# Kernel optimization log

Hardware: AMD Instinct MI355X
Metric: run time of the kernel (lower is better)

Reference implementation:

```python
import jax, jax.numpy as jnp
import numpy as np

NUM_EXPERTS_PER_TOK = 2

def setup_inputs() -> dict:
    key = jax.random.key(0)
    k1, k2, k3, k4 = jax.random.split(key, 4)
    B, S, D, O, E = 2, 4096, 2048, 2048, 8
    x = jax.random.normal(k1, (B, S, D), dtype=jnp.float32)
    gate_w = jax.random.normal(k2, (E, D), dtype=jnp.float32) * 0.02
    expert_w = jax.random.normal(k3, (E, O, D), dtype=jnp.float32) * 0.02
    expert_b = jax.random.normal(k4, (E, O), dtype=jnp.float32) * 0.02
    return {"x": x, "gate_w": gate_w, "expert_w": expert_w, "expert_b": expert_b}

def reference(x, gate_w, expert_w, expert_b):
    E = gate_w.shape[0]
    O = expert_w.shape[1]
    # Router: gate logits [B,S,E], top-k selection, softmax over the k logits (fp32 then cast)
    gate_logits = jnp.einsum('bsd,ed->bse', x, gate_w)
    topk_vals, topk_idx = jax.lax.top_k(gate_logits, NUM_EXPERTS_PER_TOK)
    weights = jax.nn.softmax(topk_vals.astype(jnp.float32), axis=-1).astype(x.dtype)
    # Dense combine weights [B,S,E]: weight of expert e for each token (0 if not selected)
    dense_w = jnp.sum(jax.nn.one_hot(topk_idx, E, dtype=x.dtype) * weights[..., None], axis=2)
    # Per-expert linear + weighted combine (loop over small fixed E)
    out = jnp.zeros(x.shape[:2] + (O,), dtype=x.dtype)
    for e in range(E):
        y_e = jnp.einsum('bsd,od->bso', x, expert_w[e]) + expert_b[e]
        out = out + dense_w[..., e:e + 1] * y_e
    return out
```

## Files before the change

### kernel.cpp

```cpp
#include <hip/hip_runtime.h>
#include <stdint.h>
#include <math.h>

#define T_TOK 8192
#define DIM   2048
#define OUTD  2048
#define NEXP  8
#define NKT   (DIM / 32)

typedef __bf16 bf16x8 __attribute__((ext_vector_type(8)));
typedef float  f32x4  __attribute__((ext_vector_type(4)));

__device__ __forceinline__ unsigned short f2bf(float f) {
  union { float f; uint32_t u; } c = {f};
  uint32_t r = (c.u + 0x7FFFu + ((c.u >> 16) & 1u)) >> 16;
  return (unsigned short)r;
}
__device__ __forceinline__ float bf2f(unsigned short h) {
  union { uint32_t u; float f; } c = {((uint32_t)h) << 16};
  return c.f;
}

__device__ __forceinline__ void gld_lds16(const void* g, void* l) {
  auto gp = reinterpret_cast<const __attribute__((address_space(1))) char*>(
      reinterpret_cast<uintptr_t>(g));
  auto lp = reinterpret_cast<__attribute__((address_space(3))) char*>(
      reinterpret_cast<uintptr_t>(l));
  __builtin_amdgcn_global_load_lds(gp, lp, 16, 0, 0);
}

__global__ __launch_bounds__(256) void split_hi_lo(const float* __restrict__ src,
                                                   unsigned short* __restrict__ hi,
                                                   unsigned short* __restrict__ lo,
                                                   int n4) {
  int stride = gridDim.x * blockDim.x;
  for (int i = blockIdx.x * blockDim.x + threadIdx.x; i < n4; i += stride) {
    float4 v = reinterpret_cast<const float4*>(src)[i];
    ushort4 h, l;
    h.x = f2bf(v.x); l.x = f2bf(v.x - bf2f(h.x));
    h.y = f2bf(v.y); l.y = f2bf(v.y - bf2f(h.y));
    h.z = f2bf(v.z); l.z = f2bf(v.z - bf2f(h.z));
    h.w = f2bf(v.w); l.w = f2bf(v.w - bf2f(h.w));
    reinterpret_cast<ushort4*>(hi)[i] = h;
    reinterpret_cast<ushort4*>(lo)[i] = l;
  }
}

__global__ __launch_bounds__(256) void router_split(const float* __restrict__ x,
                                                    const float* __restrict__ gw,
                                                    unsigned short* __restrict__ xh,
                                                    unsigned short* __restrict__ xl,
                                                    int* __restrict__ cnt,
                                                    int* __restrict__ tok_list,
                                                    float* __restrict__ tok_w) {
  const int t    = blockIdx.x * 4 + (threadIdx.x >> 6);
  const int lane = threadIdx.x & 63;
  const float4* xr = reinterpret_cast<const float4*>(x + (size_t)t * DIM);
  ushort4* xhr = reinterpret_cast<ushort4*>(xh + (size_t)t * DIM);
  ushort4* xlr = reinterpret_cast<ushort4*>(xl + (size_t)t * DIM);
  double acc[NEXP];
#pragma unroll
  for (int e = 0; e < NEXP; ++e) acc[e] = 0.0;
#pragma unroll
  for (int i = 0; i < DIM / (4 * 64); ++i) {
    float4 xv = xr[i * 64 + lane];
    ushort4 h, l;
    h.x = f2bf(xv.x); l.x = f2bf(xv.x - bf2f(h.x));
    h.y = f2bf(xv.y); l.y = f2bf(xv.y - bf2f(h.y));
    h.z = f2bf(xv.z); l.z = f2bf(xv.z - bf2f(h.z));
    h.w = f2bf(xv.w); l.w = f2bf(xv.w - bf2f(h.w));
    xhr[i * 64 + lane] = h;
    xlr[i * 64 + lane] = l;
#pragma unroll
    for (int e = 0; e < NEXP; ++e) {
      float4 gv = reinterpret_cast<const float4*>(gw + e * DIM)[i * 64 + lane];
      acc[e] += (double)xv.x * gv.x + (double)xv.y * gv.y +
                (double)xv.z * gv.z + (double)xv.w * gv.w;
    }
  }
#pragma unroll
  for (int off = 32; off >= 1; off >>= 1)
#pragma unroll
    for (int e = 0; e < NEXP; ++e) acc[e] += __shfl_down(acc[e], off, 64);
  if (lane == 0) {
    float lg[NEXP];
#pragma unroll
    for (int e = 0; e < NEXP; ++e) lg[e] = (float)acc[e];
    int i0 = 0; float v0 = lg[0];
    int i1 = -1; float v1 = -3.4e38f;
#pragma unroll
    for (int e = 1; e < NEXP; ++e) {
      if (lg[e] > v0)      { i1 = i0; v1 = v0; i0 = e; v0 = lg[e]; }
      else if (lg[e] > v1) { i1 = e;  v1 = lg[e]; }
    }
    float p  = expf(v1 - v0);
    float w0 = 1.0f / (1.0f + p);
    float w1 = p * w0;
    int s0 = atomicAdd(&cnt[i0], 1);
    tok_list[i0 * T_TOK + s0] = t; tok_w[i0 * T_TOK + s0] = w0;
    int s1 = atomicAdd(&cnt[i1], 1);
    tok_list[i1 * T_TOK + s1] = t; tok_w[i1 * T_TOK + s1] = w1;
  }
}

__global__ __launch_bounds__(512, 2) void moe_gemm(
    const unsigned short* __restrict__ xh, const unsigned short* __restrict__ xl,
    const unsigned short* __restrict__ wh, const unsigned short* __restrict__ wl,
    const float* __restrict__ eb,
    const int* __restrict__ cnt,
    const int* __restrict__ tok_list, const float* __restrict__ tok_w,
    float* __restrict__ out) {
  const int gid = blockIdx.x;
  const int by  = gid & 7;
  const int rb  = gid >> 3;
  int e = 0, off = 0, ce = 0;
#pragma unroll
  for (int ee = 0; ee < NEXP; ++ee) {
    int c  = cnt[ee];
    int nb = (c + 255) >> 8;
    if (rb >= off && rb < off + nb && ce == 0) { e = ee; ce = c; }
    off += (rb >= off + nb && ce == 0) ? nb : 0;
  }
  if (ce == 0) return;
  const int bx = rb - off;

  const int tid = threadIdx.x;
  const int l   = tid & 63;
  const int w   = tid >> 6;
  const int wr  = w >> 2, wc = w & 3;

  extern __shared__ char smem[];
  int*   stok = reinterpret_cast<int*>(smem + 131072);
  float* sw   = reinterpret_cast<float*>(smem + 132096);

  if (tid < 256) {
    int rg = bx * 256 + tid;
    bool v = rg < ce;
    stok[tid] = v ? tok_list[e * T_TOK + rg] : 0;
    sw[tid]   = v ? tok_w[e * T_TOK + rg]   : 0.0f;
  }
  __syncthreads();

  const unsigned short* asrc[4];
  const unsigned short* bsrc[4];
#pragma unroll
  for (int i = 0; i < 4; ++i) {
    int g = i * 512 + tid;
    int r = g >> 3, p = g & 7, s = p ^ (r & 7);
    asrc[i] = (s < 4 ? xh : xl) + (size_t)stok[r] * DIM + (s & 3) * 8;
    bsrc[i] = (s < 4 ? wh : wl) + ((size_t)e * OUTD + by * 256 + r) * DIM + (s & 3) * 8;
  }

  const int ph = (l >> 4) ^ (l & 7);
  const int pl = ((l >> 4) + 4) ^ (l & 7);
  const int aOh = (wr * 128 + (l & 15)) * 128 + ph * 16;
  const int aOl = (wr * 128 + (l & 15)) * 128 + pl * 16;
  const int bOh = 32768 + (wc * 64 + (l & 15)) * 128 + ph * 16;
  const int bOl = 32768 + (wc * 64 + (l & 15)) * 128 + pl * 16;

  f32x4 acc[8][4] = {};

  auto STAGE = [&](int buf, int kk) {
    char* base = smem + buf * 65536;
#pragma unroll
    for (int i = 0; i < 4; ++i) {
      gld_lds16(asrc[i] + kk, base + tid * 16 + i * 8192);
      gld_lds16(bsrc[i] + kk, base + 32768 + tid * 16 + i * 8192);
    }
  };

  STAGE(0, 0);

  for (int kt = 0; kt < NKT; ++kt) {
    const int cur = kt & 1;
    if (kt + 1 < NKT) {
      STAGE(cur ^ 1, (kt + 1) * 32);
      asm volatile("s_waitcnt vmcnt(8)" ::: "memory");
    } else {
      asm volatile("s_waitcnt vmcnt(0)" ::: "memory");
    }
    __builtin_amdgcn_s_barrier();
    __builtin_amdgcn_sched_barrier(0);

    char* b = smem + cur * 65536;
    bf16x8 bh[4], bl[4];
#pragma unroll
    for (int n = 0; n < 4; ++n) {
      bh[n] = *reinterpret_cast<const bf16x8*>(b + bOh + n * 2048);
      bl[n] = *reinterpret_cast<const bf16x8*>(b + bOl + n * 2048);
    }
#pragma unroll
    for (int m = 0; m < 8; ++m) {
      bf16x8 ah = *reinterpret_cast<const bf16x8*>(b + aOh + m * 2048);
      bf16x8 al = *reinterpret_cast<const bf16x8*>(b + aOl + m * 2048);
#pragma unroll
      for (int n = 0; n < 4; ++n) {
        acc[m][n] = __builtin_amdgcn_mfma_f32_16x16x32_bf16(ah, bh[n], acc[m][n], 0, 0, 0);
        acc[m][n] = __builtin_amdgcn_mfma_f32_16x16x32_bf16(ah, bl[n], acc[m][n], 0, 0, 0);
        acc[m][n] = __builtin_amdgcn_mfma_f32_16x16x32_bf16(al, bh[n], acc[m][n], 0, 0, 0);
      }
    }
    __builtin_amdgcn_sched_barrier(0);
    __builtin_amdgcn_s_barrier();
  }

#pragma unroll
  for (int n = 0; n < 4; ++n) {
    const int gc = by * 256 + wc * 64 + n * 16 + (l & 15);
    const float bias = eb[e * OUTD + gc];
#pragma unroll
    for (int m = 0; m < 8; ++m) {
      const int r = wr * 128 + m * 16 + (l >> 4) * 4;
#pragma unroll
      for (int q = 0; q < 4; ++q) {
        int   tk = stok[r + q];
        float wt = sw[r + q];
        float val = wt * (acc[m][n][q] + bias);
        atomicAdd(out + (size_t)tk * OUTD + gc, val);
      }
    }
  }
}

__attribute__((constructor)) static void set_lds_attr() {
  hipFuncSetAttribute((const void*)moe_gemm,
                      hipFuncAttributeMaxDynamicSharedMemorySize, 133120);
}

extern "C" void kernel_launch(void* const* d_in, const int* in_sizes, int n_in,
                              void* d_out, int out_size, void* d_ws, size_t ws_size,
                              hipStream_t stream) {
  const float* x  = (const float*)d_in[0];
  const float* gw = (const float*)d_in[1];
  const float* ew = (const float*)d_in[2];
  const float* eb = (const float*)d_in[3];
  float* out = (float*)d_out;

  char* ws = (char*)d_ws;
  int*   cnt      = (int*)(ws);
  int*   tok_list = (int*)(ws + 256);
  float* tok_w    = (float*)(ws + 256 + 262144);
  unsigned short* xh = (unsigned short*)(ws + 524544);
  unsigned short* xl = xh + 16777216;
  unsigned short* wh = xl + 16777216;
  unsigned short* wl = wh + 33554432;

  hipMemsetAsync(cnt, 0, 256, stream);
  hipMemsetAsync(d_out, 0, (size_t)out_size * sizeof(float), stream);

  split_hi_lo<<<4096, 256, 0, stream>>>(ew, wh, wl, 33554432 / 4);
  router_split<<<T_TOK / 4, 256, 0, stream>>>(x, gw, xh, xl, cnt, tok_list, tok_w);

  moe_gemm<<<dim3(576), 512, 133120, stream>>>(xh, xl, wh, wl, eb, cnt,
                                               tok_list, tok_w, out);
}
```

Measured before the change: 1.080 ms.

## Enlarge MoE GEMM row tile to 288 and software-pipeline A-fragment LDS loads

Changes the per-block token tile from 256 to 288 rows (9 m-fragments per wave), shrinking the grid from 576 to 512 blocks so the per-expert work maps more evenly onto the CUs. Global-to-LDS staging now uses 32-bit offsets from one workspace base, and the inner loop prefetches A fragments two steps ahead, with s_setprio raising wave priority around the MFMA bursts. This adds accumulator registers and LDS use (about 141 KB per block), which may reduce occupancy, and the uneven per-wave load count needs different vmcnt waits.

After: 1.014 ms. 6.1% less time.

```diff
diff --git a/kernel.cpp b/kernel.cpp
--- a/kernel.cpp
+++ b/kernel.cpp
@@ -7,6 +7,8 @@
 #define OUTD  2048
 #define NEXP  8
 #define NKT   (DIM / 32)
+#define BM    288
+#define NGRAN (BM * 8 + 2048)
 
 typedef __bf16 bf16x8 __attribute__((ext_vector_type(8)));
 typedef float  f32x4  __attribute__((ext_vector_type(4)));
@@ -117,7 +119,7 @@
 #pragma unroll
   for (int ee = 0; ee < NEXP; ++ee) {
     int c  = cnt[ee];
-    int nb = (c + 255) >> 8;
+    int nb = (c + (BM - 1)) / BM;
     if (rb >= off && rb < off + nb && ce == 0) { e = ee; ce = c; }
     off += (rb >= off + nb && ce == 0) ? nb : 0;
   }
@@ -130,42 +132,52 @@
   const int wr  = w >> 2, wc = w & 3;
 
   extern __shared__ char smem[];
-  int*   stok = reinterpret_cast<int*>(smem + 131072);
-  float* sw   = reinterpret_cast<float*>(smem + 132096);
-
-  if (tid < 256) {
-    int rg = bx * 256 + tid;
+  int*   stok = reinterpret_cast<int*>(smem + 139264);
+  float* sw   = reinterpret_cast<float*>(smem + 140416);
+
+  if (tid < BM) {
+    int rg = bx * BM + tid;
     bool v = rg < ce;
     stok[tid] = v ? tok_list[e * T_TOK + rg] : 0;
     sw[tid]   = v ? tok_w[e * T_TOK + rg]   : 0.0f;
   }
   __syncthreads();
 
-  const unsigned short* asrc[4];
-  const unsigned short* bsrc[4];
-#pragma unroll
-  for (int i = 0; i < 4; ++i) {
+  const char* wsbase = (const char*)xh;
+  uint32_t goff[9];
+#pragma unroll
+  for (int i = 0; i < 9; ++i) {
     int g = i * 512 + tid;
-    int r = g >> 3, p = g & 7, s = p ^ (r & 7);
-    asrc[i] = (s < 4 ? xh : xl) + (size_t)stok[r] * DIM + (s & 3) * 8;
-    bsrc[i] = (s < 4 ? wh : wl) + ((size_t)e * OUTD + by * 256 + r) * DIM + (s & 3) * 8;
-  }
-
-  const int ph = (l >> 4) ^ (l & 7);
-  const int pl = ((l >> 4) + 4) ^ (l & 7);
-  const int aOh = (wr * 128 + (l & 15)) * 128 + ph * 16;
-  const int aOl = (wr * 128 + (l & 15)) * 128 + pl * 16;
-  const int bOh = 32768 + (wc * 64 + (l & 15)) * 128 + ph * 16;
-  const int bOl = 32768 + (wc * 64 + (l & 15)) * 128 + pl * 16;
-
-  f32x4 acc[8][4] = {};
-
-  auto STAGE = [&](int buf, int kk) {
-    char* base = smem + buf * 65536;
-#pragma unroll
-    for (int i = 0; i < 4; ++i) {
-      gld_lds16(asrc[i] + kk, base + tid * 16 + i * 8192);
-      gld_lds16(bsrc[i] + kk, base + 32768 + tid * 16 + i * 8192);
+    if (g < BM * 8) {
+      int r = g >> 3, p = g & 7, s = p ^ (r & 7);
+      goff[i] = (s < 4 ? 0u : 33554432u) +
+                ((uint32_t)stok[r] * DIM + (s & 3) * 8) * 2u;
+    } else if (g < NGRAN) {
+      int gb = g - BM * 8;
+      int r = gb >> 3, p = gb & 7, s = p ^ (r & 7);
+      goff[i] = (s < 4 ? 67108864u : 134217728u) +
+                (((uint32_t)e * OUTD + by * 256 + r) * DIM + (s & 3) * 8) * 2u;
+    } else goff[i] = 0;
+  }
+  __syncthreads();
+
+  const int ph  = (l >> 4) ^ (l & 7);
+  const int pl  = ((l >> 4) + 4) ^ (l & 7);
+  const int aOh = (wr * 144 + (l & 15)) * 128 + ph * 16;
+  const int aOl = (wr * 144 + (l & 15)) * 128 + pl * 16;
+  const int bOh = 36864 + (wc * 64 + (l & 15)) * 128 + ph * 16;
+  const int bOl = 36864 + (wc * 64 + (l & 15)) * 128 + pl * 16;
+
+  f32x4 acc[9][4] = {};
+
+  auto STAGE = [&](int buf, int kt1) {
+    char* base = smem + buf * 69632 + tid * 16;
+    const char* gb = wsbase + kt1 * 64;
+#pragma unroll
+    for (int i = 0; i < 9; ++i) {
+      int g = i * 512 + tid;
+      if (g < NGRAN)
+        gld_lds16(gb + goff[i], base + i * 8192);
     }
   };
 
@@ -174,32 +186,48 @@
   for (int kt = 0; kt < NKT; ++kt) {
     const int cur = kt & 1;
     if (kt + 1 < NKT) {
-      STAGE(cur ^ 1, (kt + 1) * 32);
-      asm volatile("s_waitcnt vmcnt(8)" ::: "memory");
+      STAGE(cur ^ 1, kt + 1);
+      if (w < 4) asm volatile("s_waitcnt vmcnt(9)" ::: "memory");
+      else       asm volatile("s_waitcnt vmcnt(8)" ::: "memory");
     } else {
       asm volatile("s_waitcnt vmcnt(0)" ::: "memory");
     }
     __builtin_amdgcn_s_barrier();
     __builtin_amdgcn_sched_barrier(0);
 
-    char* b = smem + cur * 65536;
-    bf16x8 bh[4], bl[4];
+    const char* b = smem + cur * 69632;
+    auto LD = [&](int o) { return *reinterpret_cast<const bf16x8*>(b + o); };
+
+    bf16x8 bhv[4], blv[4];
 #pragma unroll
     for (int n = 0; n < 4; ++n) {
-      bh[n] = *reinterpret_cast<const bf16x8*>(b + bOh + n * 2048);
-      bl[n] = *reinterpret_cast<const bf16x8*>(b + bOl + n * 2048);
-    }
-#pragma unroll
-    for (int m = 0; m < 8; ++m) {
-      bf16x8 ah = *reinterpret_cast<const bf16x8*>(b + aOh + m * 2048);
-      bf16x8 al = *reinterpret_cast<const bf16x8*>(b + aOl + m * 2048);
+      bhv[n] = LD(bOh + n * 2048);
+      blv[n] = LD(bOl + n * 2048);
+    }
+    auto MM = [&](bf16x8 ah, bf16x8 al, int m) {
 #pragma unroll
       for (int n = 0; n < 4; ++n) {
-        acc[m][n] = __builtin_amdgcn_mfma_f32_16x16x32_bf16(ah, bh[n], acc[m][n], 0, 0, 0);
-        acc[m][n] = __builtin_amdgcn_mfma_f32_16x16x32_bf16(ah, bl[n], acc[m][n], 0, 0, 0);
-        acc[m][n] = __builtin_amdgcn_mfma_f32_16x16x32_bf16(al, bh[n], acc[m][n], 0, 0, 0);
+        acc[m][n] = __builtin_amdgcn_mfma_f32_16x16x32_bf16(ah, bhv[n], acc[m][n], 0, 0, 0);
+        acc[m][n] = __builtin_amdgcn_mfma_f32_16x16x32_bf16(ah, blv[n], acc[m][n], 0, 0, 0);
+        acc[m][n] = __builtin_amdgcn_mfma_f32_16x16x32_bf16(al, bhv[n], acc[m][n], 0, 0, 0);
       }
-    }
+    };
+
+    bf16x8 c0h = LD(aOh),            c0l = LD(aOl);
+    bf16x8 c1h = LD(aOh + 2048),     c1l = LD(aOl + 2048);
+    bf16x8 n0h = LD(aOh + 2 * 2048), n0l = LD(aOl + 2 * 2048);
+    bf16x8 n1h = LD(aOh + 3 * 2048), n1l = LD(aOl + 3 * 2048);
+    __builtin_amdgcn_s_setprio(1); MM(c0h, c0l, 0); MM(c1h, c1l, 1); __builtin_amdgcn_s_setprio(0);
+    c0h = LD(aOh + 4 * 2048); c0l = LD(aOl + 4 * 2048);
+    c1h = LD(aOh + 5 * 2048); c1l = LD(aOl + 5 * 2048);
+    __builtin_amdgcn_s_setprio(1); MM(n0h, n0l, 2); MM(n1h, n1l, 3); __builtin_amdgcn_s_setprio(0);
+    n0h = LD(aOh + 6 * 2048); n0l = LD(aOl + 6 * 2048);
+    n1h = LD(aOh + 7 * 2048); n1l = LD(aOl + 7 * 2048);
+    __builtin_amdgcn_s_setprio(1); MM(c0h, c0l, 4); MM(c1h, c1l, 5); __builtin_amdgcn_s_setprio(0);
+    c0h = LD(aOh + 8 * 2048); c0l = LD(aOl + 8 * 2048);
+    __builtin_amdgcn_s_setprio(1); MM(n0h, n0l, 6); MM(n1h, n1l, 7); __builtin_amdgcn_s_setprio(0);
+    __builtin_amdgcn_s_setprio(1); MM(c0h, c0l, 8); __builtin_amdgcn_s_setprio(0);
+
     __builtin_amdgcn_sched_barrier(0);
     __builtin_amdgcn_s_barrier();
   }
@@ -209,8 +237,8 @@
     const int gc = by * 256 + wc * 64 + n * 16 + (l & 15);
     const float bias = eb[e * OUTD + gc];
 #pragma unroll
-    for (int m = 0; m < 8; ++m) {
-      const int r = wr * 128 + m * 16 + (l >> 4) * 4;
+    for (int m = 0; m < 9; ++m) {
+      const int r = wr * 144 + m * 16 + (l >> 4) * 4;
 #pragma unroll
       for (int q = 0; q < 4; ++q) {
         int   tk = stok[r + q];
@@ -224,7 +252,7 @@
 
 __attribute__((constructor)) static void set_lds_attr() {
   hipFuncSetAttribute((const void*)moe_gemm,
-                      hipFuncAttributeMaxDynamicSharedMemorySize, 133120);
+                      hipFuncAttributeMaxDynamicSharedMemorySize, 141568);
 }
 
 extern "C" void kernel_launch(void* const* d_in, const int* in_sizes, int n_in,
@@ -251,6 +279,6 @@
   split_hi_lo<<<4096, 256, 0, stream>>>(ew, wh, wl, 33554432 / 4);
   router_split<<<T_TOK / 4, 256, 0, stream>>>(x, gw, xh, xl, cnt, tok_list, tok_w);
 
-  moe_gemm<<<dim3(576), 512, 133120, stream>>>(xh, xl, wh, wl, eb, cnt,
+  moe_gemm<<<dim3(512), 512, 141568, stream>>>(xh, xl, wh, wl, eb, cnt,
                                                tok_list, tok_w, out);
 }
```
